# Kernel optimization log

Measured on AMD Instinct MI355X. Metric: run time of the kernel, lower is better.

## Reference

```python
import jax, jax.numpy as jnp
import numpy as np

NEG = -1e30  # log-space 'zero'


def _lse3(a, b, c):
    m = jnp.maximum(jnp.maximum(a, b), c)
    return m + jnp.log(jnp.exp(a - m) + jnp.exp(b - m) + jnp.exp(c - m))


def _ctc_loss_sum(logp, targets, input_lens, target_lens, blank=0):
    # logp: (T, B, C) log-probabilities; targets: (B, S) int; lens: (B,) int
    T, B, C = logp.shape
    S = targets.shape[1]
    L = 2 * S + 1
    # Extended label sequence: blank, t0, blank, t1, ..., blank  -> (B, L)
    ext = jnp.full((B, L), blank, dtype=targets.dtype).at[:, 1::2].set(targets)
    # Skip transition (l-2 -> l) allowed only for non-blank labels differing from l-2
    allow_skip = jnp.concatenate(
        [jnp.zeros((B, 2), bool), (ext[:, 2:] != blank) & (ext[:, 2:] != ext[:, :-2])],
        axis=1)  # (B, L)
    pos = jnp.arange(L)[None, :]
    valid = pos < (2 * target_lens[:, None] + 1)  # (B, L) mask of used trellis columns

    def emit(lp_t):  # (B, C) -> (B, L): log-prob of emitting ext label at each position
        return jnp.take_along_axis(lp_t, ext, axis=1)

    e0 = emit(logp[0])
    alpha0 = jnp.full((B, L), NEG, logp.dtype).at[:, 0].set(e0[:, 0]).at[:, 1].set(e0[:, 1])
    alpha0 = jnp.where(valid, alpha0, NEG)

    def step(alpha, lp_t):
        a1 = jnp.pad(alpha[:, :-1], ((0, 0), (1, 0)), constant_values=NEG)
        a2 = jnp.pad(alpha[:, :-2], ((0, 0), (2, 0)), constant_values=NEG)
        a2 = jnp.where(allow_skip, a2, NEG)
        new = _lse3(alpha, a1, a2) + emit(lp_t)
        new = jnp.where(valid, new, NEG)
        return new, new

    _, alphas = jax.lax.scan(step, alpha0, logp[1:])
    alphas = jnp.concatenate([alpha0[None], alphas], axis=0)  # (T, B, L)

    # Per-sequence final alpha at t = input_len - 1
    a_fin = alphas[input_lens - 1, jnp.arange(B)]  # (B, L)
    end_blank = jnp.take_along_axis(a_fin, (2 * target_lens)[:, None], axis=1)[:, 0]
    end_label = jnp.take_along_axis(a_fin, (2 * target_lens - 1)[:, None], axis=1)[:, 0]
    m = jnp.maximum(end_blank, end_label)
    loss = -(m + jnp.log(jnp.exp(end_blank - m) + jnp.exp(end_label - m)))  # (B,)
    # zero_infinity=True: replace (near-)infinite losses with 0
    loss = jnp.where(loss > -0.5 * NEG, 0.0, loss)
    # reduction='none' followed by .sum() in the module
    return loss.sum()


def setup_inputs() -> dict:
    key = jax.random.key(0)
    T, B, C, S = 1000, 32, 1000, 100
    k1, k2 = jax.random.split(key)
    logits = jax.random.normal(k1, (T, B, C), dtype=jnp.float32)
    logp = jax.nn.log_softmax(logits, axis=-1)  # CTCLoss expects log-softmax input
    targets = jax.random.randint(k2, (B, S), 1, C)  # labels in [1, C), never blank(0)
    input_lens = jnp.full((B,), T, dtype=jnp.int32)
    target_lens = jnp.full((B,), S, dtype=jnp.int32)
    return {"logp": logp, "targets": targets, "input_lens": input_lens, "target_lens": target_lens}


def reference(logp, targets, input_lens, target_lens):
    return _ctc_loss_sum(logp, targets, input_lens, target_lens, blank=0)
```

## Files before the change

### kernel.cpp

```cpp
#include <hip/hip_runtime.h>
#include <hip/hip_fp16.h>


constexpr int T = 1000, B = 32, C = 1000, S = 100;
constexpr int L = 2 * S + 1;
constexpr int RS = 204;
constexpr int PFD = 32;
constexpr int RROWS = T + PFD;
constexpr float OFF = 7.0f;
constexpr float LOG2E = 1.4426950408889634f;
constexpr float LN2 = 0.6931471805599453f;

__device__ __forceinline__ float dpp_shr1(float x) {
    return __int_as_float(
        __builtin_amdgcn_update_dpp(0, __float_as_int(x), 0x138, 0xF, 0xF, true));
}

__device__ __forceinline__ float wave_max_nonneg(float x) {
#define DPP_MAX(ctrl)                                                        \
    x = fmaxf(x, __int_as_float(__builtin_amdgcn_update_dpp(                 \
                     0, __float_as_int(x), (ctrl), 0xF, 0xF, true)))
    DPP_MAX(0x111);
    DPP_MAX(0x112);
    DPP_MAX(0x114);
    DPP_MAX(0x118);
    DPP_MAX(0x142);
    DPP_MAX(0x143);
#undef DPP_MAX
    return __int_as_float(__builtin_amdgcn_readlane(__float_as_int(x), 63));
}

__device__ __forceinline__ void h4_to_f(const uint2 q, float& x, float& y,
                                        float& z, float& w) {
    const __half2 lo = *reinterpret_cast<const __half2*>(&q.x);
    const __half2 hi = *reinterpret_cast<const __half2*>(&q.y);
    const float2 f01 = __half22float2(lo);
    const float2 f23 = __half22float2(hi);
    x = f01.x; y = f01.y; z = f23.x; w = f23.y;
}

__global__ void stage_kernel(const float* __restrict__ logp,
                             const int* __restrict__ targets,
                             __half* __restrict__ ws) {
    const int t = blockIdx.x;
    const int b = blockIdx.y;
    __shared__ float row[C];
    const float* src = logp + ((size_t)t * B + b) * C;
    const int tid = threadIdx.x;
    if (tid < C / 4) {
        ((float4*)row)[tid] = ((const float4*)src)[tid];
    }
    __syncthreads();
    if (tid < RS) {
        float p;
        if (tid < L) {
            const int c = (tid & 1) ? targets[b * S + (tid >> 1)] : 0;
            p = exp2f((row[c] + OFF) * LOG2E);
        } else {
            p = 0.0f;
        }
        ws[((size_t)b * RROWS + t) * RS + tid] = __float2half(p);
    }
}

__global__ void __launch_bounds__(64, 1) ctc_kernel(
        const __half* __restrict__ ws, const int* __restrict__ targets,
        const int* __restrict__ input_lens, const int* __restrict__ target_lens,
        float* __restrict__ out) {
    const int b = blockIdx.x;
    const int lane = threadIdx.x;
    const int col = (lane <= 50) ? 4 * lane : 200;
    const int Tb = input_lens[b];
    const int tl = target_lens[b];
    const __half* pw = ws + (size_t)b * RROWS * RS;

    float m1 = 0.f, m3 = 0.f;
    if (lane <= 50) {
        const int l1 = col + 1;
        if (l1 >= 3 && l1 < L) {
            const int s = (l1 - 1) >> 1;
            if (targets[b * S + s] != targets[b * S + s - 1]) m1 = 1.f;
        }
        const int l3 = col + 3;
        if (l3 >= 3 && l3 < L) {
            const int s = (l3 - 1) >> 1;
            if (targets[b * S + s] != targets[b * S + s - 1]) m3 = 1.f;
        }
    }

    float a0 = 0.f, a1 = 0.f, a2 = 0.f, a3 = 0.f;
    {
        const uint2 q0 = *(const uint2*)(pw + col);
        float x, y, z, w;
        h4_to_f(q0, x, y, z, w);
        if (lane == 0) { a0 = x; a1 = y; }
    }
    int esum = 0;

#define CTC_STEP(Q_)                                  \
    do {                                              \
        float px, py, pz, pwv;                        \
        h4_to_f((Q_), px, py, pz, pwv);               \
        const float am1 = dpp_shr1(a3);               \
        const float s01 = a0 + a1;                    \
        const float s23 = a2 + a3;                    \
        const float n0 = (a0 + am1) * px;             \
        const float n1 = fmaf(am1, m1, s01) * py;     \
        const float n2 = (a1 + a2) * pz;              \
        const float n3 = fmaf(a1, m3, s23) * pwv;     \
        a0 = n0; a1 = n1; a2 = n2; a3 = n3;           \
    } while (0)

#define CTC_RESCALE()                                                          \
    do {                                                                       \
        const float mx = wave_max_nonneg(fmaxf(fmaxf(a0, a1), fmaxf(a2, a3))); \
        const unsigned bits = __float_as_uint(mx);                             \
        if (bits != 0u) {                                                      \
            const int e = (int)((bits >> 23) & 0xFFu) - 127;                   \
            const float sc = __uint_as_float((unsigned)(127 - e) << 23);       \
            a0 *= sc; a1 *= sc; a2 *= sc; a3 *= sc;                            \
            esum += e;                                                         \
        }                                                                      \
    } while (0)

    uint2 P[PFD];
    {
        const __half* pf0 = pw + (size_t)RS + col;
#pragma unroll
        for (int i = 0; i < PFD; ++i) P[i] = *(const uint2*)(pf0 + (size_t)i * RS);
    }
    const __half* pf = pw + (size_t)(PFD + 1) * RS + col;

    int t = 1;
    while (t + PFD <= Tb) {
#pragma unroll
        for (int i = 0; i < PFD; ++i) {
            const uint2 q = P[i];
            P[i] = *(const uint2*)pf;
            pf += RS;
            CTC_STEP(q);
            if (i == 15) CTC_RESCALE();
        }
        CTC_RESCALE();
        t += PFD;
    }
    {
        const int rem = Tb - t;
#pragma unroll
        for (int i = 0; i < PFD; ++i) {
            if (i < rem) {
                const uint2 q = P[i];
                CTC_STEP(q);
                if (i == 15) CTC_RESCALE();
            }
        }
    }
#undef CTC_STEP

    const int e1 = 2 * tl, e2 = 2 * tl - 1;
    float contrib = 0.f;
    if (lane <= 50) {
        if (col + 0 == e1 || col + 0 == e2) contrib += a0;
        if (col + 1 == e1 || col + 1 == e2) contrib += a1;
        if (col + 2 == e1 || col + 2 == e2) contrib += a2;
        if (col + 3 == e1 || col + 3 == e2) contrib += a3;
    }
#pragma unroll
    for (int off = 32; off; off >>= 1) contrib += __shfl_xor(contrib, off);

    if (lane == 0) {
        const float logalpha = logf(contrib) + (float)esum * LN2 - OFF * (float)Tb;
        float loss = -logalpha;
        if (!(loss < 0.5e30f)) loss = 0.f;
        atomicAdd(out, loss);
    }
}

__global__ void __launch_bounds__(64, 1) ctc_direct_kernel(
        const float* __restrict__ logp, const int* __restrict__ targets,
        const int* __restrict__ input_lens, const int* __restrict__ target_lens,
        float* __restrict__ out) {
    const int b = blockIdx.x;
    const int lane = threadIdx.x;
    const int col = (lane <= 50) ? 4 * lane : 200;
    const int Tb = input_lens[b];
    const int tl = target_lens[b];

    int cc[4]; float mm[4], pm[4];
#pragma unroll
    for (int i = 0; i < 4; ++i) {
        const int l = col + i;
        const bool real = (lane <= 50) && (l < L);
        pm[i] = real ? 1.f : 0.f;
        cc[i] = real ? ((l & 1) ? targets[b * S + (l >> 1)] : 0) : 0;
        float mk = 0.f;
        if (real && (l & 1) && l >= 3) {
            const int s = (l - 1) >> 1;
            if (targets[b * S + s] != targets[b * S + s - 1]) mk = 1.f;
        }
        mm[i] = mk;
    }
    const float m1 = mm[1], m3 = mm[3];

    float a0 = 0.f, a1 = 0.f, a2 = 0.f, a3 = 0.f;
    {
        const float* rowp = logp + (size_t)b * C;
        const float p0 = pm[0] * exp2f((rowp[cc[0]] + OFF) * LOG2E);
        const float p1 = pm[1] * exp2f((rowp[cc[1]] + OFF) * LOG2E);
        if (lane == 0) { a0 = p0; a1 = p1; }
    }
    int esum = 0;

    for (int t = 1; t < Tb; ++t) {
        const float* rowp = logp + ((size_t)t * B + b) * C;
        const float p0 = pm[0] * exp2f((rowp[cc[0]] + OFF) * LOG2E);
        const float p1 = pm[1] * exp2f((rowp[cc[1]] + OFF) * LOG2E);
        const float p2 = pm[2] * exp2f((rowp[cc[2]] + OFF) * LOG2E);
        const float p3 = pm[3] * exp2f((rowp[cc[3]] + OFF) * LOG2E);
        const float am1 = dpp_shr1(a3);
        const float n0 = (a0 + am1) * p0;
        const float n1 = fmaf(am1, m1, a0 + a1) * p1;
        const float n2 = (a1 + a2) * p2;
        const float n3 = fmaf(a1, m3, a2 + a3) * p3;
        a0 = n0; a1 = n1; a2 = n2; a3 = n3;
        if ((t & 15) == 0) {
            const float mx = wave_max_nonneg(fmaxf(fmaxf(a0, a1), fmaxf(a2, a3)));
            const unsigned bits = __float_as_uint(mx);
            if (bits != 0u) {
                const int e = (int)((bits >> 23) & 0xFFu) - 127;
                const float sc = __uint_as_float((unsigned)(127 - e) << 23);
                a0 *= sc; a1 *= sc; a2 *= sc; a3 *= sc;
                esum += e;
            }
        }
    }

    const int e1 = 2 * tl, e2 = 2 * tl - 1;
    float contrib = 0.f;
    if (lane <= 50) {
        if (col + 0 == e1 || col + 0 == e2) contrib += a0;
        if (col + 1 == e1 || col + 1 == e2) contrib += a1;
        if (col + 2 == e1 || col + 2 == e2) contrib += a2;
        if (col + 3 == e1 || col + 3 == e2) contrib += a3;
    }
#pragma unroll
    for (int off = 32; off; off >>= 1) contrib += __shfl_xor(contrib, off);
    if (lane == 0) {
        const float logalpha = logf(contrib) + (float)esum * LN2 - OFF * (float)Tb;
        float loss = -logalpha;
        if (!(loss < 0.5e30f)) loss = 0.f;
        atomicAdd(out, loss);
    }
}

extern "C" void kernel_launch(void* const* d_in, const int* in_sizes, int n_in,
                              void* d_out, int out_size, void* d_ws, size_t ws_size,
                              hipStream_t stream) {
    const float* logp = (const float*)d_in[0];
    const int* targets = (const int*)d_in[1];
    const int* input_lens = (const int*)d_in[2];
    const int* target_lens = (const int*)d_in[3];
    float* out = (float*)d_out;
    __half* ws = (__half*)d_ws;

    hipMemsetAsync(d_out, 0, sizeof(float), stream);

    const size_t ws_needed = (size_t)B * RROWS * RS * sizeof(__half);
    if (ws_size >= ws_needed) {
        dim3 gA(T, B);
        stage_kernel<<<gA, 256, 0, stream>>>(logp, targets, ws);
        ctc_kernel<<<B, 64, 0, stream>>>(ws, targets, input_lens, target_lens, out);
    } else {
        ctc_direct_kernel<<<B, 64, 0, stream>>>(logp, targets, input_lens, target_lens, out);
    }
}
```

Measured before the change: 234.7 us.

## Fuse staging into CTC kernel with producer waves double-buffering emissions in LDS

Replaces the two-kernel pipeline (a staging kernel that writes half-precision emission probabilities to a global workspace, then a single-wave recurrence kernel) with one fused kernel per batch item. Fifteen producer waves gather, exponentiate and convert emission probabilities for 120-timestep chunks into a double-buffered LDS array, while wave 0 runs the alpha recurrence from LDS. This removes the workspace round trip through global memory, one kernel launch, and the full-row staging copies. In exchange it adds a block-wide barrier per chunk and occupies only 32 blocks, so latency of the scattered global gathers must be hidden by the producer waves. The LDS footprint is about 98 KB per block.

```diff
diff --git a/kernel.cpp b/kernel.cpp
--- a/kernel.cpp
+++ b/kernel.cpp
@@ -5,8 +5,9 @@
 constexpr int T = 1000, B = 32, C = 1000, S = 100;
 constexpr int L = 2 * S + 1;
 constexpr int RS = 204;
-constexpr int PFD = 32;
-constexpr int RROWS = T + PFD;
+constexpr int CHUNK = 120;
+constexpr int NPROD = 15;
+constexpr int RPP = CHUNK / NPROD;
 constexpr float OFF = 7.0f;
 constexpr float LOG2E = 1.4426950408889634f;
 constexpr float LN2 = 0.6931471805599453f;
@@ -39,40 +40,63 @@
     x = f01.x; y = f01.y; z = f23.x; w = f23.y;
 }
 
-__global__ void stage_kernel(const float* __restrict__ logp,
-                             const int* __restrict__ targets,
-                             __half* __restrict__ ws) {
-    const int t = blockIdx.x;
-    const int b = blockIdx.y;
-    __shared__ float row[C];
-    const float* src = logp + ((size_t)t * B + b) * C;
-    const int tid = threadIdx.x;
-    if (tid < C / 4) {
-        ((float4*)row)[tid] = ((const float4*)src)[tid];
-    }
-    __syncthreads();
-    if (tid < RS) {
-        float p;
-        if (tid < L) {
-            const int c = (tid & 1) ? targets[b * S + (tid >> 1)] : 0;
-            p = exp2f((row[c] + OFF) * LOG2E);
-        } else {
-            p = 0.0f;
-        }
-        ws[((size_t)b * RROWS + t) * RS + tid] = __float2half(p);
-    }
-}
-
-__global__ void __launch_bounds__(64, 1) ctc_kernel(
-        const __half* __restrict__ ws, const int* __restrict__ targets,
+__global__ void __launch_bounds__(1024) ctc_fused_kernel(
+        const float* __restrict__ logp, const int* __restrict__ targets,
         const int* __restrict__ input_lens, const int* __restrict__ target_lens,
         float* __restrict__ out) {
+    __shared__ __half lds[2][CHUNK][RS];
+
     const int b = blockIdx.x;
-    const int lane = threadIdx.x;
-    const int col = (lane <= 50) ? 4 * lane : 200;
+    const int wave = threadIdx.x >> 6;
+    const int lane = threadIdx.x & 63;
     const int Tb = input_lens[b];
     const int tl = target_lens[b];
-    const __half* pw = ws + (size_t)b * RROWS * RS;
+    const int col = (lane <= 50) ? 4 * lane : 200;
+
+    const int steps = Tb - 1;
+    const int NC = (steps + CHUNK - 1) / CHUNK;
+
+    if (wave > 0) {
+        const int p = wave - 1;
+        int cc[4];
+        float pm[4];
+#pragma unroll
+        for (int i = 0; i < 4; ++i) {
+            const int l = col + i;
+            const bool real = (lane <= 50) && (l < L);
+            pm[i] = real ? 1.f : 0.f;
+            cc[i] = real ? ((l & 1) ? targets[b * S + (l >> 1)] : 0) : 0;
+        }
+        auto produce = [&](int c, int bi) {
+            const int t0 = 1 + c * CHUNK;
+#pragma unroll 2
+            for (int rr = 0; rr < RPP; ++rr) {
+                const int r = p + rr * NPROD;
+                const int t = t0 + r;
+                if (t >= Tb) break;
+                const float* row = logp + ((size_t)t * B + b) * C;
+                const float p0 = pm[0] * exp2f((row[cc[0]] + OFF) * LOG2E);
+                const float p1 = pm[1] * exp2f((row[cc[1]] + OFF) * LOG2E);
+                const float p2 = pm[2] * exp2f((row[cc[2]] + OFF) * LOG2E);
+                const float p3 = pm[3] * exp2f((row[cc[3]] + OFF) * LOG2E);
+                if (lane <= 50) {
+                    const __half2 lo = __floats2half2_rn(p0, p1);
+                    const __half2 hi = __floats2half2_rn(p2, p3);
+                    uint2 q;
+                    q.x = *reinterpret_cast<const unsigned int*>(&lo);
+                    q.y = *reinterpret_cast<const unsigned int*>(&hi);
+                    *reinterpret_cast<uint2*>(&lds[bi][r][col]) = q;
+                }
+            }
+        };
+        if (NC > 0) produce(0, 0);
+        __syncthreads();
+        for (int c = 0; c < NC; ++c) {
+            if (c + 1 < NC) produce(c + 1, (c + 1) & 1);
+            __syncthreads();
+        }
+        return;
+    }
 
     float m1 = 0.f, m3 = 0.f;
     if (lane <= 50) {
@@ -89,11 +113,10 @@
     }
 
     float a0 = 0.f, a1 = 0.f, a2 = 0.f, a3 = 0.f;
-    {
-        const uint2 q0 = *(const uint2*)(pw + col);
-        float x, y, z, w;
-        h4_to_f(q0, x, y, z, w);
-        if (lane == 0) { a0 = x; a1 = y; }
+    if (lane == 0) {
+        const float* r0 = logp + (size_t)b * C;
+        a0 = __half2float(__float2half(exp2f((r0[0] + OFF) * LOG2E)));
+        a1 = __half2float(__float2half(exp2f((r0[targets[b * S]] + OFF) * LOG2E)));
     }
     int esum = 0;
 
@@ -123,39 +146,21 @@
         }                                                                      \
     } while (0)
 
-    uint2 P[PFD];
-    {
-        const __half* pf0 = pw + (size_t)RS + col;
-#pragma unroll
-        for (int i = 0; i < PFD; ++i) P[i] = *(const uint2*)(pf0 + (size_t)i * RS);
-    }
-    const __half* pf = pw + (size_t)(PFD + 1) * RS + col;
-
-    int t = 1;
-    while (t + PFD <= Tb) {
-#pragma unroll
-        for (int i = 0; i < PFD; ++i) {
-            const uint2 q = P[i];
-            P[i] = *(const uint2*)pf;
-            pf += RS;
+    __syncthreads();
+    for (int c = 0; c < NC; ++c) {
+        const int bi = c & 1;
+        const int t0 = 1 + c * CHUNK;
+        const int rend = min(CHUNK, Tb - t0);
+#pragma unroll 4
+        for (int r = 0; r < rend; ++r) {
+            const uint2 q = *reinterpret_cast<const uint2*>(&lds[bi][r][col]);
             CTC_STEP(q);
-            if (i == 15) CTC_RESCALE();
+            if (((t0 + r) & 15) == 0) CTC_RESCALE();
         }
-        CTC_RESCALE();
-        t += PFD;
-    }
-    {
-        const int rem = Tb - t;
-#pragma unroll
-        for (int i = 0; i < PFD; ++i) {
-            if (i < rem) {
-                const uint2 q = P[i];
-                CTC_STEP(q);
-                if (i == 15) CTC_RESCALE();
-            }
-        }
+        __syncthreads();
     }
 #undef CTC_STEP
+#undef CTC_RESCALE
 
     const int e1 = 2 * tl, e2 = 2 * tl - 1;
     float contrib = 0.f;
@@ -176,101 +181,17 @@
     }
 }
 
-__global__ void __launch_bounds__(64, 1) ctc_direct_kernel(
-        const float* __restrict__ logp, const int* __restrict__ targets,
-        const int* __restrict__ input_lens, const int* __restrict__ target_lens,
-        float* __restrict__ out) {
-    const int b = blockIdx.x;
-    const int lane = threadIdx.x;
-    const int col = (lane <= 50) ? 4 * lane : 200;
-    const int Tb = input_lens[b];
-    const int tl = target_lens[b];
-
-    int cc[4]; float mm[4], pm[4];
-#pragma unroll
-    for (int i = 0; i < 4; ++i) {
-        const int l = col + i;
-        const bool real = (lane <= 50) && (l < L);
-        pm[i] = real ? 1.f : 0.f;
-        cc[i] = real ? ((l & 1) ? targets[b * S + (l >> 1)] : 0) : 0;
-        float mk = 0.f;
-        if (real && (l & 1) && l >= 3) {
-            const int s = (l - 1) >> 1;
-            if (targets[b * S + s] != targets[b * S + s - 1]) mk = 1.f;
-        }
-        mm[i] = mk;
-    }
-    const float m1 = mm[1], m3 = mm[3];
-
-    float a0 = 0.f, a1 = 0.f, a2 = 0.f, a3 = 0.f;
-    {
-        const float* rowp = logp + (size_t)b * C;
-        const float p0 = pm[0] * exp2f((rowp[cc[0]] + OFF) * LOG2E);
-        const float p1 = pm[1] * exp2f((rowp[cc[1]] + OFF) * LOG2E);
-        if (lane == 0) { a0 = p0; a1 = p1; }
-    }
-    int esum = 0;
-
-    for (int t = 1; t < Tb; ++t) {
-        const float* rowp = logp + ((size_t)t * B + b) * C;
-        const float p0 = pm[0] * exp2f((rowp[cc[0]] + OFF) * LOG2E);
-        const float p1 = pm[1] * exp2f((rowp[cc[1]] + OFF) * LOG2E);
-        const float p2 = pm[2] * exp2f((rowp[cc[2]] + OFF) * LOG2E);
-        const float p3 = pm[3] * exp2f((rowp[cc[3]] + OFF) * LOG2E);
-        const float am1 = dpp_shr1(a3);
-        const float n0 = (a0 + am1) * p0;
-        const float n1 = fmaf(am1, m1, a0 + a1) * p1;
-        const float n2 = (a1 + a2) * p2;
-        const float n3 = fmaf(a1, m3, a2 + a3) * p3;
-        a0 = n0; a1 = n1; a2 = n2; a3 = n3;
-        if ((t & 15) == 0) {
-            const float mx = wave_max_nonneg(fmaxf(fmaxf(a0, a1), fmaxf(a2, a3)));
-            const unsigned bits = __float_as_uint(mx);
-            if (bits != 0u) {
-                const int e = (int)((bits >> 23) & 0xFFu) - 127;
-                const float sc = __uint_as_float((unsigned)(127 - e) << 23);
-                a0 *= sc; a1 *= sc; a2 *= sc; a3 *= sc;
-                esum += e;
-            }
-        }
-    }
-
-    const int e1 = 2 * tl, e2 = 2 * tl - 1;
-    float contrib = 0.f;
-    if (lane <= 50) {
-        if (col + 0 == e1 || col + 0 == e2) contrib += a0;
-        if (col + 1 == e1 || col + 1 == e2) contrib += a1;
-        if (col + 2 == e1 || col + 2 == e2) contrib += a2;
-        if (col + 3 == e1 || col + 3 == e2) contrib += a3;
-    }
-#pragma unroll
-    for (int off = 32; off; off >>= 1) contrib += __shfl_xor(contrib, off);
-    if (lane == 0) {
-        const float logalpha = logf(contrib) + (float)esum * LN2 - OFF * (float)Tb;
-        float loss = -logalpha;
-        if (!(loss < 0.5e30f)) loss = 0.f;
-        atomicAdd(out, loss);
-    }
-}
-
 extern "C" void kernel_launch(void* const* d_in, const int* in_sizes, int n_in,
                               void* d_out, int out_size, void* d_ws, size_t ws_size,
                               hipStream_t stream) {
+    (void)d_ws; (void)ws_size; (void)in_sizes; (void)n_in; (void)out_size;
     const float* logp = (const float*)d_in[0];
     const int* targets = (const int*)d_in[1];
     const int* input_lens = (const int*)d_in[2];
     const int* target_lens = (const int*)d_in[3];
     float* out = (float*)d_out;
-    __half* ws = (__half*)d_ws;
 
     hipMemsetAsync(d_out, 0, sizeof(float), stream);
-
-    const size_t ws_needed = (size_t)B * RROWS * RS * sizeof(__half);
-    if (ws_size >= ws_needed) {
-        dim3 gA(T, B);
-        stage_kernel<<<gA, 256, 0, stream>>>(logp, targets, ws);
-        ctc_kernel<<<B, 64, 0, stream>>>(ws, targets, input_lens, target_lens, out);
-    } else {
-        ctc_direct_kernel<<<B, 64, 0, stream>>>(logp, targets, input_lens, target_lens, out);
-    }
+    ctc_fused_kernel<<<B, 1024, 0, stream>>>(logp, targets, input_lens,
+                                             target_lens, out);
 }
```

Measured after the change: 293.8 us. 1.25x slower.

## Stage emission probs in fp32 with direct gathers, one wave per timestep

Applied to the files above, without the earlier changes.

The staging kernel no longer copies the whole 1000-float row into shared memory. Each wave now gathers only the blank and target entries it needs from global memory and writes a float4 per lane, four timesteps per block. The workspace changes from half to float, which removes the half-to-float conversions from the serial recurrence and avoids fp16 precision loss. In exchange the workspace doubles in size and the recurrence kernel loads twice the bytes per step, which raises register pressure for the 32-deep prefetch buffer and may turn the workspace-size check toward the fallback path.

```diff
diff --git a/kernel.cpp b/kernel.cpp
--- a/kernel.cpp
+++ b/kernel.cpp
@@ -30,41 +30,33 @@
     return __int_as_float(__builtin_amdgcn_readlane(__float_as_int(x), 63));
 }
 
-__device__ __forceinline__ void h4_to_f(const uint2 q, float& x, float& y,
-                                        float& z, float& w) {
-    const __half2 lo = *reinterpret_cast<const __half2*>(&q.x);
-    const __half2 hi = *reinterpret_cast<const __half2*>(&q.y);
-    const float2 f01 = __half22float2(lo);
-    const float2 f23 = __half22float2(hi);
-    x = f01.x; y = f01.y; z = f23.x; w = f23.y;
-}
-
-__global__ void stage_kernel(const float* __restrict__ logp,
-                             const int* __restrict__ targets,
-                             __half* __restrict__ ws) {
-    const int t = blockIdx.x;
+__global__ void __launch_bounds__(256) stage_kernel(
+        const float* __restrict__ logp, const int* __restrict__ targets,
+        float* __restrict__ ws) {
+    const int t = blockIdx.x * 4 + (threadIdx.x >> 6);
     const int b = blockIdx.y;
-    __shared__ float row[C];
-    const float* src = logp + ((size_t)t * B + b) * C;
-    const int tid = threadIdx.x;
-    if (tid < C / 4) {
-        ((float4*)row)[tid] = ((const float4*)src)[tid];
-    }
-    __syncthreads();
-    if (tid < RS) {
-        float p;
-        if (tid < L) {
-            const int c = (tid & 1) ? targets[b * S + (tid >> 1)] : 0;
-            p = exp2f((row[c] + OFF) * LOG2E);
-        } else {
-            p = 0.0f;
-        }
-        ws[((size_t)b * RROWS + t) * RS + tid] = __float2half(p);
-    }
+    const int lane = threadIdx.x & 63;
+    if (lane > 50) return;
+    const int col = 4 * lane;
+    const float* row = logp + ((size_t)t * B + b) * C;
+
+    const float pb = exp2f((row[0] + OFF) * LOG2E);
+    float p1 = 0.f, p3 = 0.f;
+    const int l1 = col + 1;
+    if (l1 < L) p1 = exp2f((row[targets[b * S + (l1 >> 1)]] + OFF) * LOG2E);
+    const int l3 = col + 3;
+    if (l3 < L) p3 = exp2f((row[targets[b * S + (l3 >> 1)]] + OFF) * LOG2E);
+
+    float4 v;
+    v.x = pb;
+    v.y = p1;
+    v.z = (col + 2 < L) ? pb : 0.f;
+    v.w = p3;
+    *reinterpret_cast<float4*>(ws + ((size_t)b * RROWS + t) * RS + col) = v;
 }
 
 __global__ void __launch_bounds__(64, 1) ctc_kernel(
-        const __half* __restrict__ ws, const int* __restrict__ targets,
+        const float* __restrict__ ws, const int* __restrict__ targets,
         const int* __restrict__ input_lens, const int* __restrict__ target_lens,
         float* __restrict__ out) {
     const int b = blockIdx.x;
@@ -72,7 +64,7 @@
     const int col = (lane <= 50) ? 4 * lane : 200;
     const int Tb = input_lens[b];
     const int tl = target_lens[b];
-    const __half* pw = ws + (size_t)b * RROWS * RS;
+    const float* pw = ws + (size_t)b * RROWS * RS;
 
     float m1 = 0.f, m3 = 0.f;
     if (lane <= 50) {
@@ -90,24 +82,20 @@
 
     float a0 = 0.f, a1 = 0.f, a2 = 0.f, a3 = 0.f;
     {
-        const uint2 q0 = *(const uint2*)(pw + col);
-        float x, y, z, w;
-        h4_to_f(q0, x, y, z, w);
-        if (lane == 0) { a0 = x; a1 = y; }
+        const float4 q0 = *reinterpret_cast<const float4*>(pw + col);
+        if (lane == 0) { a0 = q0.x; a1 = q0.y; }
     }
     int esum = 0;
 
 #define CTC_STEP(Q_)                                  \
     do {                                              \
-        float px, py, pz, pwv;                        \
-        h4_to_f((Q_), px, py, pz, pwv);               \
         const float am1 = dpp_shr1(a3);               \
         const float s01 = a0 + a1;                    \
         const float s23 = a2 + a3;                    \
-        const float n0 = (a0 + am1) * px;             \
-        const float n1 = fmaf(am1, m1, s01) * py;     \
-        const float n2 = (a1 + a2) * pz;              \
-        const float n3 = fmaf(a1, m3, s23) * pwv;     \
+        const float n0 = (a0 + am1) * (Q_).x;         \
+        const float n1 = fmaf(am1, m1, s01) * (Q_).y; \
+        const float n2 = (a1 + a2) * (Q_).z;          \
+        const float n3 = fmaf(a1, m3, s23) * (Q_).w;  \
         a0 = n0; a1 = n1; a2 = n2; a3 = n3;           \
     } while (0)
 
@@ -123,20 +111,21 @@
         }                                                                      \
     } while (0)
 
-    uint2 P[PFD];
-    {
-        const __half* pf0 = pw + (size_t)RS + col;
-#pragma unroll
-        for (int i = 0; i < PFD; ++i) P[i] = *(const uint2*)(pf0 + (size_t)i * RS);
-    }
-    const __half* pf = pw + (size_t)(PFD + 1) * RS + col;
+    float4 P[PFD];
+    {
+        const float* pf0 = pw + (size_t)RS + col;
+#pragma unroll
+        for (int i = 0; i < PFD; ++i)
+            P[i] = *reinterpret_cast<const float4*>(pf0 + (size_t)i * RS);
+    }
+    const float* pf = pw + (size_t)(PFD + 1) * RS + col;
 
     int t = 1;
     while (t + PFD <= Tb) {
 #pragma unroll
         for (int i = 0; i < PFD; ++i) {
-            const uint2 q = P[i];
-            P[i] = *(const uint2*)pf;
+            const float4 q = P[i];
+            P[i] = *reinterpret_cast<const float4*>(pf);
             pf += RS;
             CTC_STEP(q);
             if (i == 15) CTC_RESCALE();
@@ -149,7 +138,7 @@
 #pragma unroll
         for (int i = 0; i < PFD; ++i) {
             if (i < rem) {
-                const uint2 q = P[i];
+                const float4 q = P[i];
                 CTC_STEP(q);
                 if (i == 15) CTC_RESCALE();
             }
@@ -256,21 +245,23 @@
 extern "C" void kernel_launch(void* const* d_in, const int* in_sizes, int n_in,
                               void* d_out, int out_size, void* d_ws, size_t ws_size,
                               hipStream_t stream) {
+    (void)in_sizes; (void)n_in; (void)out_size;
     const float* logp = (const float*)d_in[0];
     const int* targets = (const int*)d_in[1];
     const int* input_lens = (const int*)d_in[2];
     const int* target_lens = (const int*)d_in[3];
     float* out = (float*)d_out;
-    __half* ws = (__half*)d_ws;
+    float* ws = (float*)d_ws;
 
     hipMemsetAsync(d_out, 0, sizeof(float), stream);
 
-    const size_t ws_needed = (size_t)B * RROWS * RS * sizeof(__half);
+    const size_t ws_needed = (size_t)B * RROWS * RS * sizeof(float);
     if (ws_size >= ws_needed) {
-        dim3 gA(T, B);
+        dim3 gA(T / 4, B);
         stage_kernel<<<gA, 256, 0, stream>>>(logp, targets, ws);
         ctc_kernel<<<B, 64, 0, stream>>>(ws, targets, input_lens, target_lens, out);
     } else {
-        ctc_direct_kernel<<<B, 64, 0, stream>>>(logp, targets, input_lens, target_lens, out);
-    }
-}
+        ctc_direct_kernel<<<B, 64, 0, stream>>>(logp, targets, input_lens,
+                                                target_lens, out);
+    }
+}
```

New measurement: 234.9 us. No clear change (+0.1%).
